# Kernel optimization log

Hardware: AMD Instinct MI355X
Metric: run time of the kernel (lower is better)

The kernel has to match this reference:

```python
import jax, jax.numpy as jnp
import numpy as np

N = 100000      # num_nodes
E = 400000      # num edges
HID = 128       # hidden_channels (== in_channels, memory dim)
OUT = 64        # out_channels (per head)
HEADS = 4
HD = HEADS * OUT  # 256, TransformerConv concat output dim


def _lin(k, fan_in, fan_out):
    return jax.random.normal(k, (fan_in, fan_out), jnp.float32) * 0.02


def setup_inputs() -> dict:
    key = jax.random.key(0)
    ks = jax.random.split(key, 16)
    return {
        "edge_index": jax.random.randint(ks[0], (2, E), 0, N, dtype=jnp.int64),
        "edge_time": jax.random.randint(ks[1], (E, 1), 0, 1000000, dtype=jnp.int64),
        "x": jax.random.normal(ks[2], (N, HID), jnp.float32),
        "memory": jax.random.normal(ks[3], (N, HID), jnp.float32),  # TGN memory table (detached in fwd)
        # TransformerConv params (lin_query / lin_key / lin_value / lin_skip, all with bias)
        "Wq": _lin(ks[4], HID, HD), "bq": jnp.zeros((HD,), jnp.float32),
        "Wk": _lin(ks[5], HID, HD), "bk": jnp.zeros((HD,), jnp.float32),
        "Wv": _lin(ks[6], HID, HD), "bv": jnp.zeros((HD,), jnp.float32),
        "Wskip": _lin(ks[7], HID, HD), "bskip": jnp.zeros((HD,), jnp.float32),
        # rating MLP: Linear(512,128) -> ReLU -> Linear(128,64) -> ReLU -> Linear(64,1)
        "W1": _lin(ks[8], 2 * HD, 128), "b1": jnp.zeros((128,), jnp.float32),
        "W2": _lin(ks[9], 128, 64), "b2": jnp.zeros((64,), jnp.float32),
        "W3": _lin(ks[10], 64, 1), "b3": jnp.zeros((1,), jnp.float32),
    }


def reference(edge_index, edge_time, x, memory,
              Wq, bq, Wk, bk, Wv, bv, Wskip, bskip,
              W1, b1, W2, b2, W3, b3):
    src, dst = edge_index[0], edge_index[1]
    n = x.shape[0]

    # x = memory.detach() + x
    h = memory + x  # [N, HID]

    # TransformerConv (heads=4, concat=True, root_weight=True)
    q = (h @ Wq + bq).reshape(n, HEADS, OUT)
    k = (h @ Wk + bk).reshape(n, HEADS, OUT)
    v = (h @ Wv + bv).reshape(n, HEADS, OUT)

    # per-edge attention scores: messages flow src -> dst, softmax over in-edges of dst
    scores = jnp.sum(q[dst] * k[src], axis=-1) / jnp.sqrt(jnp.float32(OUT))  # [E, H]
    smax = jax.ops.segment_max(scores, dst, num_segments=n)                   # [N, H]
    e = jnp.exp(scores - smax[dst])
    denom = jax.ops.segment_sum(e, dst, num_segments=n)
    alpha = e / (denom[dst] + 1e-16)                                          # [E, H]

    agg = jax.ops.segment_sum(alpha[:, :, None] * v[src], dst, num_segments=n)  # [N, H, OUT]
    out = agg.reshape(n, HD) + (h @ Wskip + bskip)                              # skip connection

    # interaction embeddings + MLP head (dropout inactive at eval)
    inter = jnp.concatenate([out[src], out[dst]], axis=-1)  # [E, 512]
    hdd = jax.nn.relu(inter @ W1 + b1)
    hdd = jax.nn.relu(hdd @ W2 + b2)
    rating = jax.nn.sigmoid(hdd @ W3 + b3) * 4.0 + 1.0
    return rating[:, 0]
```

## Files before the change

### kernel.cpp

```cpp
#include <hip/hip_runtime.h>
#include <math.h>

#define N_NODES 100000
#define N_EDGES 400000
#define HID 128
#define HEADS 4
#define OUT_C 64
#define HD 256
#define SCAN_CHUNK 1024
#define NB_SCAN ((N_NODES + SCAN_CHUNK - 1) / SCAN_CHUNK)

typedef __attribute__((ext_vector_type(8))) short bf16x8;
typedef __attribute__((ext_vector_type(4))) float f32x4;

__device__ __forceinline__ unsigned short fbf(float f) {
    unsigned u = __float_as_uint(f);
    unsigned r = (u + 0x7fffu + ((u >> 16) & 1u)) >> 16;
    return (unsigned short)r;
}
__device__ __forceinline__ float bf2f(unsigned short u) {
    return __uint_as_float(((unsigned)u) << 16);
}

__device__ __forceinline__ void gl_lds16(const void* g, void* l) {
    __builtin_amdgcn_global_load_lds(
        (const __attribute__((address_space(1))) unsigned int*)g,
        (__attribute__((address_space(3))) unsigned int*)l,
        16, 0, 0);
}

__global__ __launch_bounds__(256) void init_zero(int* __restrict__ deg,
                                                 int* __restrict__ cursor) {
    int i = blockIdx.x * 256 + threadIdx.x;
    if (i < N_NODES) { deg[i] = 0; cursor[i] = 0; }
}

__global__ __launch_bounds__(256) void k_deg(const int* __restrict__ ei,
                                             int* __restrict__ deg) {
    int e = blockIdx.x * 256 + threadIdx.x;
    if (e < N_EDGES) atomicAdd(&deg[ei[N_EDGES + e]], 1);
}

__global__ __launch_bounds__(256) void k_scan1(const int* __restrict__ deg,
                                               int* __restrict__ rp,
                                               int* __restrict__ bsum) {
    __shared__ int ts[256];
    int b = blockIdx.x, t = threadIdx.x;
    int base = b * SCAN_CHUNK + t * 4;
    int vv[4];
    int s = 0;
#pragma unroll
    for (int i = 0; i < 4; ++i) {
        int d = (base + i < N_NODES) ? deg[base + i] : 0;
        vv[i] = s;
        s += d;
    }
    ts[t] = s;
    __syncthreads();
    for (int off = 1; off < 256; off <<= 1) {
        int x = (t >= off) ? ts[t - off] : 0;
        __syncthreads();
        ts[t] += x;
        __syncthreads();
    }
    int ex = ts[t] - s;
#pragma unroll
    for (int i = 0; i < 4; ++i)
        if (base + i < N_NODES) rp[base + i] = ex + vv[i];
    if (t == 255) bsum[b] = ts[255];
}

__global__ __launch_bounds__(256) void k_scan2(int* __restrict__ bsum) {
    __shared__ int ts[256];
    int t = threadIdx.x;
    int v = (t < NB_SCAN) ? bsum[t] : 0;
    ts[t] = v;
    __syncthreads();
    for (int off = 1; off < 256; off <<= 1) {
        int x = (t >= off) ? ts[t - off] : 0;
        __syncthreads();
        ts[t] += x;
        __syncthreads();
    }
    if (t < NB_SCAN) bsum[t] = ts[t] - v;
}

__global__ __launch_bounds__(256) void k_scan3(int* __restrict__ rp,
                                               const int* __restrict__ bsum) {
    int i = blockIdx.x * 256 + threadIdx.x;
    if (i < N_NODES) rp[i] += bsum[i / SCAN_CHUNK];
}

__global__ __launch_bounds__(256) void k_bucket(const int* __restrict__ ei,
                                                const int* __restrict__ rp,
                                                int* __restrict__ cursor,
                                                int* __restrict__ csr_src,
                                                int* __restrict__ csr_dst,
                                                int* __restrict__ csr_eid) {
    int e = blockIdx.x * 256 + threadIdx.x;
    if (e >= N_EDGES) return;
    int src = ei[e];
    int d   = ei[N_EDGES + e];
    int idx = atomicAdd(&cursor[d], 1);
    int s   = rp[d] + idx;
    csr_src[s] = src;
    csr_dst[s] = d;
    csr_eid[s] = e;
}

__global__ __launch_bounds__(256) void pack_wg(
    const float* __restrict__ Wq, const float* __restrict__ Wk,
    const float* __restrict__ Wv, const float* __restrict__ Ws,
    unsigned short* __restrict__ Wp) {
    int i = blockIdx.x * 256 + threadIdx.x;
    if (i >= 16384) return;
    int lane = i & 63, nt = (i >> 6) & 15, kt = (i >> 10) & 3, z = i >> 12;
    const float* W = (z == 0) ? Wq : (z == 1) ? Wk : (z == 2) ? Wv : Ws;
    int q = lane >> 4, c = lane & 15;
#pragma unroll
    for (int j = 0; j < 8; ++j)
        Wp[i * 8 + j] = fbf(W[(kt * 32 + q * 8 + j) * HD + nt * 16 + c]);
}

__global__ __launch_bounds__(256) void pack_wc(const float* __restrict__ W1,
                                               unsigned short* __restrict__ Wcp) {
    int i = blockIdx.x * 256 + threadIdx.x;
    if (i >= 8192) return;
    int lane = i & 63, nt = (i >> 6) & 15, kt = i >> 10;
    int q = lane >> 4, c = lane & 15;
    int n = nt * 16 + c;
#pragma unroll
    for (int j = 0; j < 8; ++j) {
        int k = kt * 32 + q * 8 + j;
        float v = (n < 128) ? W1[k * 128 + n] : W1[(k + 256) * 128 + (n - 128)];
        Wcp[i * 8 + j] = fbf(v);
    }
}

__global__ __launch_bounds__(256) void pack_w2(const float* __restrict__ W2,
                                               unsigned short* __restrict__ W2p) {
    int i = blockIdx.x * 256 + threadIdx.x;
    if (i >= 1024) return;
    int lane = i & 63, nt = (i >> 6) & 3, kt = i >> 8;
    int q = lane >> 4, c = lane & 15;
#pragma unroll
    for (int j = 0; j < 8; ++j)
        W2p[i * 8 + j] = fbf(W2[(kt * 32 + q * 8 + j) * 64 + nt * 16 + c]);
}

__global__ __launch_bounds__(256) void k_pre(const float* __restrict__ x,
                                             const float* __restrict__ mem,
                                             unsigned short* __restrict__ H) {
    int idx = blockIdx.x * 256 + threadIdx.x;
    if (idx >= N_NODES * HID / 8) return;
    const float4* x4 = (const float4*)x;
    const float4* m4 = (const float4*)mem;
    float4 a0 = x4[(size_t)idx * 2],     a1 = x4[(size_t)idx * 2 + 1];
    float4 b0 = m4[(size_t)idx * 2],     b1 = m4[(size_t)idx * 2 + 1];
    bf16x8 hv;
    hv[0] = (short)fbf(a0.x + b0.x); hv[1] = (short)fbf(a0.y + b0.y);
    hv[2] = (short)fbf(a0.z + b0.z); hv[3] = (short)fbf(a0.w + b0.w);
    hv[4] = (short)fbf(a1.x + b1.x); hv[5] = (short)fbf(a1.y + b1.y);
    hv[6] = (short)fbf(a1.z + b1.z); hv[7] = (short)fbf(a1.w + b1.w);
    *(bf16x8*)&H[(size_t)idx * 8] = hv;
}

__global__ __launch_bounds__(256, 4) void gemm4(
    const unsigned short* __restrict__ H,
    const unsigned short* __restrict__ Wp,
    const float* __restrict__ bq, const float* __restrict__ bk,
    const float* __restrict__ bv, const float* __restrict__ bs,
    unsigned short* __restrict__ Q, unsigned short* __restrict__ KV,
    unsigned short* __restrict__ S)
{
    __shared__ __align__(16) short sh[4 * 64 * 68];
    short* As = sh;

    const int t = threadIdx.x;
    const int w = t >> 6, l = t & 63;
    const int q = l >> 4, c = l & 15;
    const int z  = blockIdx.y;
    const int m0 = blockIdx.x * 64;

#pragma unroll
    for (int i = 0; i < 4; ++i) {
        int rbase = w * 16 + i * 4;
        int r  = rbase + (l >> 4);
        int gr = m0 + r; if (gr >= N_NODES) gr = N_NODES - 1;
        int ks = (l & 15) ^ (r & 7);
        gl_lds16(&H[(size_t)gr * HID + ks * 8], &As[rbase * 128]);
    }

    unsigned short* Oz; int rs, coff; const float* bz;
    if      (z == 0) { Oz = Q;  rs = 256; coff = 0;   bz = bq; }
    else if (z == 1) { Oz = KV; rs = 512; coff = 0;   bz = bk; }
    else if (z == 2) { Oz = KV; rs = 512; coff = 256; bz = bv; }
    else             { Oz = S;  rs = 256; coff = 0;   bz = bs; }
    float bb[4];
#pragma unroll
    for (int nt = 0; nt < 4; ++nt) bb[nt] = bz[w * 64 + nt * 16 + c];

    f32x4 acc[4][4];
#pragma unroll
    for (int mt = 0; mt < 4; ++mt)
#pragma unroll
        for (int nt = 0; nt < 4; ++nt) acc[mt][nt] = (f32x4){0.f, 0.f, 0.f, 0.f};

    __syncthreads();

#pragma unroll
    for (int kt = 0; kt < 4; ++kt) {
        bf16x8 af[4];
#pragma unroll
        for (int mt = 0; mt < 4; ++mt) {
            int row  = mt * 16 + c;
            int slot = (kt * 4 + q) ^ (row & 7);
            af[mt] = *(const bf16x8*)&As[row * 128 + slot * 8];
        }
#pragma unroll
        for (int nt = 0; nt < 4; ++nt) {
            bf16x8 bw8 = *(const bf16x8*)&Wp[(size_t)(((z * 4 + kt) * 16 + w * 4 + nt) * 64 + l) * 8];
#pragma unroll
            for (int mt = 0; mt < 4; ++mt)
                acc[mt][nt] = __builtin_amdgcn_mfma_f32_16x16x32_bf16(af[mt], bw8, acc[mt][nt], 0, 0, 0);
        }
    }
    __syncthreads();

    short* slab = &sh[w * 64 * 68];
#pragma unroll
    for (int nt = 0; nt < 4; ++nt)
#pragma unroll
        for (int mt = 0; mt < 4; ++mt)
#pragma unroll
            for (int r = 0; r < 4; ++r)
                slab[(mt * 16 + q * 4 + r) * 68 + nt * 16 + c] =
                    (short)fbf(acc[mt][nt][r] + bb[nt]);

    const int srow = l >> 3, schk = l & 7;
#pragma unroll
    for (int j = 0; j < 8; ++j) {
        int row = j * 8 + srow;
        int gr  = m0 + row;
        if (gr < N_NODES)
            *(bf16x8*)&Oz[(size_t)gr * rs + coff + w * 64 + schk * 8] =
                *(const bf16x8*)&slab[row * 68 + schk * 8];
    }
}

__global__ __launch_bounds__(256) void k_attn(
    const int* __restrict__ rp, const int* __restrict__ deg,
    const int* __restrict__ csr_src,
    const unsigned short* __restrict__ Q, const unsigned short* __restrict__ KV,
    const unsigned short* __restrict__ S,
    unsigned short* __restrict__ out)
{
    int node = blockIdx.x * 4 + (threadIdx.x >> 6);
    int l = threadIdx.x & 63;
    if (node >= N_NODES) return;
    int start = rp[node];
    int cnt   = deg[node];

    float q0, q1, q2, q3;
    {
        ushort4 u = *(const ushort4*)&Q[(size_t)node * HD + l * 4];
        q0 = bf2f(u.x); q1 = bf2f(u.y); q2 = bf2f(u.z); q3 = bf2f(u.w);
    }

    float m = -1e30f, d = 0.f;
    float a0 = 0.f, a1 = 0.f, a2 = 0.f, a3 = 0.f;

    for (int i = 0; i < cnt; ++i) {
        int src = csr_src[start + i];
        const unsigned short* kv = &KV[(size_t)src * 512 + l * 4];
        ushort4 ku = *(const ushort4*)kv;
        ushort4 vu = *(const ushort4*)(kv + 256);
        float s = q0 * bf2f(ku.x) + q1 * bf2f(ku.y) + q2 * bf2f(ku.z) + q3 * bf2f(ku.w);
        s += __shfl_xor(s, 1);
        s += __shfl_xor(s, 2);
        s += __shfl_xor(s, 4);
        s += __shfl_xor(s, 8);
        s *= 0.125f;

        float mn    = fmaxf(m, s);
        float scale = __expf(m - mn);
        float e     = __expf(s - mn);
        d = d * scale + e;
        a0 = a0 * scale + e * bf2f(vu.x);
        a1 = a1 * scale + e * bf2f(vu.y);
        a2 = a2 * scale + e * bf2f(vu.z);
        a3 = a3 * scale + e * bf2f(vu.w);
        m = mn;
    }

    float inv = 1.f / (d + 1e-16f);
    ushort4 su = *(const ushort4*)&S[(size_t)node * HD + l * 4];
    ushort4 ov = make_ushort4(fbf(bf2f(su.x) + a0 * inv),
                              fbf(bf2f(su.y) + a1 * inv),
                              fbf(bf2f(su.z) + a2 * inv),
                              fbf(bf2f(su.w) + a3 * inv));
    *(ushort4*)&out[(size_t)node * HD + l * 4] = ov;
}

__global__ __launch_bounds__(256) void pd_gemm(
    const unsigned short* __restrict__ outb,
    const unsigned short* __restrict__ Wcp,
    unsigned short* __restrict__ PD)
{
    __shared__ __align__(16) char sh[4 * 64 * 68 * 2];
    short* As   = (short*)sh;
    short* Slab = (short*)sh;

    const int t = threadIdx.x;
    const int w = t >> 6, l = t & 63;
    const int q = l >> 4, c = l & 15;
    const int m0 = blockIdx.x * 64;

#pragma unroll
    for (int j = 0; j < 8; ++j) {
        int idx = t + j * 256;
        int row = idx >> 5, c4 = idx & 31;
        int gr  = m0 + row;
        bf16x8 v = (bf16x8){0,0,0,0,0,0,0,0};
        if (gr < N_NODES)
            v = *(const bf16x8*)&outb[(size_t)gr * HD + c4 * 8];
        *(bf16x8*)&As[row * 264 + c4 * 8] = v;
    }
    __syncthreads();

    f32x4 acc[4][4];
#pragma unroll
    for (int mt = 0; mt < 4; ++mt)
#pragma unroll
        for (int nt = 0; nt < 4; ++nt) acc[mt][nt] = (f32x4){0.f, 0.f, 0.f, 0.f};

#pragma unroll
    for (int kt = 0; kt < 8; ++kt) {
        bf16x8 af[4];
#pragma unroll
        for (int mt = 0; mt < 4; ++mt)
            af[mt] = *(const bf16x8*)&As[(mt * 16 + c) * 264 + kt * 32 + q * 8];
#pragma unroll
        for (int nt = 0; nt < 4; ++nt) {
            int ntg = w * 4 + nt;
            bf16x8 bv8 = *(const bf16x8*)&Wcp[(size_t)((kt * 16 + ntg) * 64 + l) * 8];
#pragma unroll
            for (int mt = 0; mt < 4; ++mt)
                acc[mt][nt] = __builtin_amdgcn_mfma_f32_16x16x32_bf16(af[mt], bv8, acc[mt][nt], 0, 0, 0);
        }
    }
    __syncthreads();

    short* slab = &Slab[w * 64 * 68];
#pragma unroll
    for (int nt = 0; nt < 4; ++nt)
#pragma unroll
        for (int mt = 0; mt < 4; ++mt)
#pragma unroll
            for (int r = 0; r < 4; ++r)
                slab[(mt * 16 + q * 4 + r) * 68 + nt * 16 + c] =
                    (short)fbf(acc[mt][nt][r]);
    const int srow = l >> 3, schk = l & 7;
#pragma unroll
    for (int j = 0; j < 8; ++j) {
        int row = j * 8 + srow;
        int gr = m0 + row;
        if (gr < N_NODES)
            *(bf16x8*)&PD[(size_t)gr * HD + w * 64 + schk * 8] =
                *(const bf16x8*)&slab[row * 68 + schk * 8];
    }
}

__global__ __launch_bounds__(256) void edge_mlp_pd(
    const int* __restrict__ csr_src, const int* __restrict__ csr_dst,
    const int* __restrict__ csr_eid,
    const unsigned short* __restrict__ PD,
    const float* __restrict__ b1,
    const unsigned short* __restrict__ W2p, const float* __restrict__ b2,
    const float* __restrict__ W3, const float* __restrict__ b3,
    float* __restrict__ rating)
{
    __shared__ __align__(16) char lds[64 * 136 * 2];
    short* h1t = (short*)lds;
    float* h2s = (float*)lds;

    const int t = threadIdx.x;
    const int w = t >> 6, l = t & 63;
    const int q = l >> 4, c = l & 15;
    const int e0 = blockIdx.x * 64;

#pragma unroll
    for (int j = 0; j < 4; ++j) {
        int idx = t + j * 256;
        int row = idx >> 4, ch = idx & 15;
        int src = csr_src[e0 + row];
        int dst = csr_dst[e0 + row];
        bf16x8 pv = *(const bf16x8*)&PD[(size_t)src * HD + ch * 8];
        bf16x8 dv = *(const bf16x8*)&PD[(size_t)dst * HD + 128 + ch * 8];
        float4 ba = *(const float4*)&b1[ch * 8];
        float4 bb = *(const float4*)&b1[ch * 8 + 4];
        bf16x8 hv;
        hv[0] = (short)fbf(fmaxf(bf2f((unsigned short)pv[0]) + bf2f((unsigned short)dv[0]) + ba.x, 0.f));
        hv[1] = (short)fbf(fmaxf(bf2f((unsigned short)pv[1]) + bf2f((unsigned short)dv[1]) + ba.y, 0.f));
        hv[2] = (short)fbf(fmaxf(bf2f((unsigned short)pv[2]) + bf2f((unsigned short)dv[2]) + ba.z, 0.f));
        hv[3] = (short)fbf(fmaxf(bf2f((unsigned short)pv[3]) + bf2f((unsigned short)dv[3]) + ba.w, 0.f));
        hv[4] = (short)fbf(fmaxf(bf2f((unsigned short)pv[4]) + bf2f((unsigned short)dv[4]) + bb.x, 0.f));
        hv[5] = (short)fbf(fmaxf(bf2f((unsigned short)pv[5]) + bf2f((unsigned short)dv[5]) + bb.y, 0.f));
        hv[6] = (short)fbf(fmaxf(bf2f((unsigned short)pv[6]) + bf2f((unsigned short)dv[6]) + bb.z, 0.f));
        hv[7] = (short)fbf(fmaxf(bf2f((unsigned short)pv[7]) + bf2f((unsigned short)dv[7]) + bb.w, 0.f));
        *(bf16x8*)&h1t[row * 136 + ch * 8] = hv;
    }
    __syncthreads();

    f32x4 acc2[4];
#pragma unroll
    for (int i = 0; i < 4; ++i) acc2[i] = (f32x4){0.f, 0.f, 0.f, 0.f};
#pragma unroll
    for (int kt = 0; kt < 4; ++kt) {
        bf16x8 av = *(const bf16x8*)&h1t[(w * 16 + c) * 136 + kt * 32 + q * 8];
#pragma unroll
        for (int nt = 0; nt < 4; ++nt) {
            bf16x8 bv = *(const bf16x8*)&W2p[(size_t)((kt * 4 + nt) * 64 + l) * 8];
            acc2[nt] = __builtin_amdgcn_mfma_f32_16x16x32_bf16(av, bv, acc2[nt], 0, 0, 0);
        }
    }
    __syncthreads();

#pragma unroll
    for (int nt = 0; nt < 4; ++nt) {
        float bv = b2[nt * 16 + c];
#pragma unroll
        for (int r = 0; r < 4; ++r)
            h2s[(w * 16 + q * 4 + r) * 65 + nt * 16 + c] = fmaxf(acc2[nt][r] + bv, 0.f);
    }
    __syncthreads();

    if (t < 64) {
        float a = b3[0];
#pragma unroll 8
        for (int kk = 0; kk < 64; ++kk)
            a += h2s[t * 65 + kk] * W3[kk];
        rating[csr_eid[e0 + t]] = 4.f / (1.f + __expf(-a)) + 1.f;
    }
}

extern "C" void kernel_launch(void* const* d_in, const int* in_sizes, int n_in,
                              void* d_out, int out_size, void* d_ws, size_t ws_size,
                              hipStream_t stream) {
    const int*   ei  = (const int*)d_in[0];
    const float* x   = (const float*)d_in[2];
    const float* mem = (const float*)d_in[3];
    const float* Wq  = (const float*)d_in[4];
    const float* bq  = (const float*)d_in[5];
    const float* Wk  = (const float*)d_in[6];
    const float* bk  = (const float*)d_in[7];
    const float* Wv  = (const float*)d_in[8];
    const float* bv  = (const float*)d_in[9];
    const float* Ws  = (const float*)d_in[10];
    const float* bs  = (const float*)d_in[11];
    const float* W1  = (const float*)d_in[12];
    const float* b1  = (const float*)d_in[13];
    const float* W2  = (const float*)d_in[14];
    const float* b2  = (const float*)d_in[15];
    const float* W3  = (const float*)d_in[16];
    const float* b3  = (const float*)d_in[17];
    float* rating = (float*)d_out;

    unsigned short* Q = (unsigned short*)d_ws;
    const size_t NHDe = (size_t)N_NODES * HD;
    unsigned short* KV = Q + NHDe;
    unsigned short* S  = KV + 2 * NHDe;
    unsigned short* H  = S + NHDe;
    int* rp      = (int*)(H + (size_t)N_NODES * HID);
    int* deg     = rp + N_NODES;
    int* cursor  = deg + N_NODES;
    int* csr_src = cursor + N_NODES;
    int* csr_dst = csr_src + N_EDGES;
    int* csr_eid = csr_dst + N_EDGES;
    int* bsum    = csr_eid + N_EDGES;
    unsigned short* Wp  = (unsigned short*)(bsum + 128);
    unsigned short* Wcp = Wp + 16384 * 8;
    unsigned short* W2p = Wcp + 8192 * 8;
    unsigned short* PD  = KV;

    const int nblk  = (N_NODES + 255) / 256;
    const int eblk  = (N_EDGES + 255) / 256;
    const int wgrid = (N_NODES + 3) / 4;
    const int pblk  = (N_NODES * HID / 8 + 255) / 256;

    init_zero<<<nblk, 256, 0, stream>>>(deg, cursor);
    k_deg<<<eblk, 256, 0, stream>>>(ei, deg);
    k_scan1<<<NB_SCAN, 256, 0, stream>>>(deg, rp, bsum);
    k_scan2<<<1, 256, 0, stream>>>(bsum);
    k_scan3<<<nblk, 256, 0, stream>>>(rp, bsum);
    k_bucket<<<eblk, 256, 0, stream>>>(ei, rp, cursor, csr_src, csr_dst, csr_eid);
    pack_wg<<<64, 256, 0, stream>>>(Wq, Wk, Wv, Ws, Wp);
    pack_wc<<<32, 256, 0, stream>>>(W1, Wcp);
    pack_w2<<<4, 256, 0, stream>>>(W2, W2p);

    k_pre<<<pblk, 256, 0, stream>>>(x, mem, H);

    gemm4<<<dim3((N_NODES + 63) / 64, 4), dim3(256), 0, stream>>>(
        H, Wp, bq, bk, bv, bs, Q, KV, S);

    k_attn<<<wgrid, 256, 0, stream>>>(rp, deg, csr_src, Q, KV, S, Q);

    pd_gemm<<<(N_NODES + 63) / 64, 256, 0, stream>>>(Q, Wcp, PD);

    edge_mlp_pd<<<N_EDGES / 64, 256, 0, stream>>>(
        csr_src, csr_dst, csr_eid, PD, b1, W2p, b2, W3, b3, rating);
}
```

Measured before the change: 429.8 us.

## Drop online-softmax max tracking, unroll edge loop, async swizzled LDS loads in pd_gemm

```diff
diff --git a/kernel.cpp b/kernel.cpp
--- a/kernel.cpp
+++ b/kernel.cpp
@@ -267,30 +267,49 @@
         q0 = bf2f(u.x); q1 = bf2f(u.y); q2 = bf2f(u.z); q3 = bf2f(u.w);
     }
 
-    float m = -1e30f, d = 0.f;
+    float d = 0.f;
     float a0 = 0.f, a1 = 0.f, a2 = 0.f, a3 = 0.f;
 
-    for (int i = 0; i < cnt; ++i) {
-        int src = csr_src[start + i];
-        const unsigned short* kv = &KV[(size_t)src * 512 + l * 4];
-        ushort4 ku = *(const ushort4*)kv;
-        ushort4 vu = *(const ushort4*)(kv + 256);
-        float s = q0 * bf2f(ku.x) + q1 * bf2f(ku.y) + q2 * bf2f(ku.z) + q3 * bf2f(ku.w);
-        s += __shfl_xor(s, 1);
-        s += __shfl_xor(s, 2);
-        s += __shfl_xor(s, 4);
-        s += __shfl_xor(s, 8);
-        s *= 0.125f;
-
-        float mn    = fmaxf(m, s);
-        float scale = __expf(m - mn);
-        float e     = __expf(s - mn);
-        d = d * scale + e;
-        a0 = a0 * scale + e * bf2f(vu.x);
-        a1 = a1 * scale + e * bf2f(vu.y);
-        a2 = a2 * scale + e * bf2f(vu.z);
-        a3 = a3 * scale + e * bf2f(vu.w);
-        m = mn;
+    int i = 0;
+    for (; i + 2 <= cnt; i += 2) {
+        int s0 = csr_src[start + i];
+        int s1 = csr_src[start + i + 1];
+        const unsigned short* kv0 = &KV[(size_t)s0 * 512 + l * 4];
+        const unsigned short* kv1 = &KV[(size_t)s1 * 512 + l * 4];
+        ushort4 ku0 = *(const ushort4*)kv0;
+        ushort4 vu0 = *(const ushort4*)(kv0 + 256);
+        ushort4 ku1 = *(const ushort4*)kv1;
+        ushort4 vu1 = *(const ushort4*)(kv1 + 256);
+        float sA = q0 * bf2f(ku0.x) + q1 * bf2f(ku0.y) + q2 * bf2f(ku0.z) + q3 * bf2f(ku0.w);
+        float sB = q0 * bf2f(ku1.x) + q1 * bf2f(ku1.y) + q2 * bf2f(ku1.z) + q3 * bf2f(ku1.w);
+        sA += __shfl_xor(sA, 1);  sB += __shfl_xor(sB, 1);
+        sA += __shfl_xor(sA, 2);  sB += __shfl_xor(sB, 2);
+        sA += __shfl_xor(sA, 4);  sB += __shfl_xor(sB, 4);
+        sA += __shfl_xor(sA, 8);  sB += __shfl_xor(sB, 8);
+        float eA = __expf(sA * 0.125f);
+        float eB = __expf(sB * 0.125f);
+        d += eA + eB;
+        a0 += eA * bf2f(vu0.x) + eB * bf2f(vu1.x);
+        a1 += eA * bf2f(vu0.y) + eB * bf2f(vu1.y);
+        a2 += eA * bf2f(vu0.z) + eB * bf2f(vu1.z);
+        a3 += eA * bf2f(vu0.w) + eB * bf2f(vu1.w);
+    }
+    if (i < cnt) {
+        int s0 = csr_src[start + i];
+        const unsigned short* kv0 = &KV[(size_t)s0 * 512 + l * 4];
+        ushort4 ku0 = *(const ushort4*)kv0;
+        ushort4 vu0 = *(const ushort4*)(kv0 + 256);
+        float sA = q0 * bf2f(ku0.x) + q1 * bf2f(ku0.y) + q2 * bf2f(ku0.z) + q3 * bf2f(ku0.w);
+        sA += __shfl_xor(sA, 1);
+        sA += __shfl_xor(sA, 2);
+        sA += __shfl_xor(sA, 4);
+        sA += __shfl_xor(sA, 8);
+        float eA = __expf(sA * 0.125f);
+        d += eA;
+        a0 += eA * bf2f(vu0.x);
+        a1 += eA * bf2f(vu0.y);
+        a2 += eA * bf2f(vu0.z);
+        a3 += eA * bf2f(vu0.w);
     }
 
     float inv = 1.f / (d + 1e-16f);
@@ -302,14 +321,13 @@
     *(ushort4*)&out[(size_t)node * HD + l * 4] = ov;
 }
 
-__global__ __launch_bounds__(256) void pd_gemm(
+__global__ __launch_bounds__(256, 4) void pd_gemm(
     const unsigned short* __restrict__ outb,
     const unsigned short* __restrict__ Wcp,
     unsigned short* __restrict__ PD)
 {
-    __shared__ __align__(16) char sh[4 * 64 * 68 * 2];
-    short* As   = (short*)sh;
-    short* Slab = (short*)sh;
+    __shared__ __align__(16) short sh[4 * 64 * 68];
+    short* As = sh;
 
     const int t = threadIdx.x;
     const int w = t >> 6, l = t & 63;
@@ -317,29 +335,31 @@
     const int m0 = blockIdx.x * 64;
 
 #pragma unroll
-    for (int j = 0; j < 8; ++j) {
-        int idx = t + j * 256;
-        int row = idx >> 5, c4 = idx & 31;
-        int gr  = m0 + row;
-        bf16x8 v = (bf16x8){0,0,0,0,0,0,0,0};
-        if (gr < N_NODES)
-            v = *(const bf16x8*)&outb[(size_t)gr * HD + c4 * 8];
-        *(bf16x8*)&As[row * 264 + c4 * 8] = v;
-    }
-    __syncthreads();
+    for (int i = 0; i < 8; ++i) {
+        int rbase = w * 16 + i * 2;
+        int r  = rbase + (l >> 5);
+        int gr = m0 + r; if (gr >= N_NODES) gr = N_NODES - 1;
+        int s  = (l & 31) ^ (r & 7);
+        gl_lds16(&outb[(size_t)gr * HD + s * 8], &As[rbase * 256]);
+    }
 
     f32x4 acc[4][4];
 #pragma unroll
     for (int mt = 0; mt < 4; ++mt)
 #pragma unroll
         for (int nt = 0; nt < 4; ++nt) acc[mt][nt] = (f32x4){0.f, 0.f, 0.f, 0.f};
+
+    __syncthreads();
 
 #pragma unroll
     for (int kt = 0; kt < 8; ++kt) {
         bf16x8 af[4];
 #pragma unroll
-        for (int mt = 0; mt < 4; ++mt)
-            af[mt] = *(const bf16x8*)&As[(mt * 16 + c) * 264 + kt * 32 + q * 8];
+        for (int mt = 0; mt < 4; ++mt) {
+            int row  = mt * 16 + c;
+            int slot = (kt * 4 + q) ^ (row & 7);
+            af[mt] = *(const bf16x8*)&As[row * 256 + slot * 8];
+        }
 #pragma unroll
         for (int nt = 0; nt < 4; ++nt) {
             int ntg = w * 4 + nt;
@@ -351,7 +371,7 @@
     }
     __syncthreads();
 
-    short* slab = &Slab[w * 64 * 68];
+    short* slab = &sh[w * 64 * 68];
 #pragma unroll
     for (int nt = 0; nt < 4; ++nt)
 #pragma unroll
```

After: 410.1 us. 4.6% less time.
